# Kernel optimization log

Hardware: AMD Instinct MI355X
Metric: run time of the kernel (lower is better)

The kernel has to match this reference:

```python
import jax, jax.numpy as jnp
import numpy as np

DIM = 2048
N_HEADS = 16
Q_RANK = 1536
KV_RANK = 512
D_NOPE = 128
D_ROPE = 64
D_V = 128
EPS = 1e-6
B, S = 2, 2048
ROPE_THETA = 10000.0


def rmsnorm(x, w, eps=EPS):
    return x * jax.lax.rsqrt(jnp.mean(x * x, axis=-1, keepdims=True) + eps) * w


def apply_rope(x):
    # x: [b, h, s, d] with d even; LLaMA-style interleaved pair rotation
    b, h, s, d = x.shape
    inv_freq = 1.0 / (ROPE_THETA ** (jnp.arange(0, d, 2, dtype=jnp.float32) / d))
    ang = jnp.arange(s, dtype=jnp.float32)[:, None] * inv_freq[None, :]  # [s, d/2]
    cos, sin = jnp.cos(ang), jnp.sin(ang)
    xr = x.reshape(b, h, s, d // 2, 2)
    x1, x2 = xr[..., 0], xr[..., 1]
    o1 = x1 * cos - x2 * sin
    o2 = x1 * sin + x2 * cos
    return jnp.stack([o1, o2], axis=-1).reshape(b, h, s, d)


def setup_inputs() -> dict:
    key = jax.random.key(0)
    ks = jax.random.split(key, 10)
    std = 0.02
    return {
        "x": jax.random.normal(ks[0], (B, S, DIM), dtype=jnp.float32),
        "wq_down": jax.random.normal(ks[1], (Q_RANK, DIM), dtype=jnp.float32) * std,
        "q_norm_w": jnp.ones((Q_RANK,), dtype=jnp.float32),
        "wq_up": jax.random.normal(ks[2], (N_HEADS * D_NOPE, Q_RANK), dtype=jnp.float32) * std,
        "wq_rope": jax.random.normal(ks[3], (N_HEADS * D_ROPE, Q_RANK), dtype=jnp.float32) * std,
        "wkv_down": jax.random.normal(ks[4], (KV_RANK, DIM), dtype=jnp.float32) * std,
        "kv_norm_w": jnp.ones((KV_RANK,), dtype=jnp.float32),
        "wkv_up": jax.random.normal(ks[5], (N_HEADS * (D_NOPE + D_V), KV_RANK), dtype=jnp.float32) * std,
        "wk_rope": jax.random.normal(ks[6], (D_ROPE, DIM), dtype=jnp.float32) * std,
        "wo": jax.random.normal(ks[7], (DIM, N_HEADS * D_V), dtype=jnp.float32) * std,
    }


def reference(x, wq_down, q_norm_w, wq_up, wq_rope, wkv_down, kv_norm_w, wkv_up, wk_rope, wo):
    bs, s, _ = x.shape
    # low-rank Q path
    q_c = rmsnorm(x @ wq_down.T, q_norm_w)                              # [b,s,qr]
    q_nope = (q_c @ wq_up.T).reshape(bs, s, N_HEADS, D_NOPE).transpose(0, 2, 1, 3)
    q_pe = (q_c @ wq_rope.T).reshape(bs, s, N_HEADS, D_ROPE).transpose(0, 2, 1, 3)
    # low-rank KV path
    kv_c = rmsnorm(x @ wkv_down.T, kv_norm_w)                           # [b,s,kvr]
    kv_up = (kv_c @ wkv_up.T).reshape(bs, s, N_HEADS, D_NOPE + D_V)
    k_nope = kv_up[..., :D_NOPE].transpose(0, 2, 1, 3)                  # [b,h,s,dn]
    v = kv_up[..., D_NOPE:].transpose(0, 2, 1, 3)                       # [b,h,s,dv]
    # shared rope key (1 head), broadcast across heads
    k_rope = (x @ wk_rope.T).reshape(bs, s, 1, D_ROPE).transpose(0, 2, 1, 3)  # [b,1,s,dr]
    q_pe = apply_rope(q_pe)
    k_rope = apply_rope(k_rope)
    q = jnp.concatenate([q_nope, q_pe], axis=-1)                        # [b,h,s,dn+dr]
    k = jnp.concatenate([k_nope, jnp.broadcast_to(k_rope, (bs, N_HEADS, s, D_ROPE))], axis=-1)
    scale = 1.0 / np.sqrt(D_NOPE + D_ROPE)
    scores = jnp.einsum('bhqd,bhkd->bhqk', q, k) * scale                # [b,h,s,s]
    causal = jnp.tril(jnp.ones((s, s), dtype=bool))
    scores = jnp.where(causal, scores, -jnp.inf)
    probs = jax.nn.softmax(scores, axis=-1)
    out = jnp.einsum('bhqk,bhkv->bhqv', probs, v)                       # [b,h,s,dv]
    out = out.transpose(0, 2, 1, 3).reshape(bs, s, N_HEADS * D_V)
    return out @ wo.T
```

## Files before the change

### kernel.cpp

```cpp
#include <hip/hip_runtime.h>
#include <stdint.h>

typedef _Float16 f16x8 __attribute__((ext_vector_type(8)));
typedef _Float16 f16x4 __attribute__((ext_vector_type(4)));
typedef float fx4 __attribute__((ext_vector_type(4)));

static constexpr int S_LEN = 2048;
static constexpr int BATCH = 2;
static constexpr int TOKENS = BATCH * S_LEN;
static constexpr int DIM = 2048;
static constexpr int NH = 16;
static constexpr int QR = 1536;
static constexpr int KVR = 512;
static constexpr int DN = 128;
static constexpr int DR = 64;
static constexpr int DV = 128;

__device__ __forceinline__ void async16(const _Float16* g, _Float16* lds_base_uniform) {
  __builtin_amdgcn_global_load_lds(
      (const __attribute__((address_space(1))) void*)g,
      (__attribute__((address_space(3))) void*)lds_base_uniform, 16, 0, 0);
}

__device__ __forceinline__ void bar() {
  asm volatile("" ::: "memory");
  __builtin_amdgcn_s_barrier();
  asm volatile("" ::: "memory");
}
#define VMWAIT(n) asm volatile("s_waitcnt vmcnt(" #n ")" ::: "memory")

#define ROR16(x, ctrl) \
  __uint_as_float(__builtin_amdgcn_update_dpp(__float_as_uint(x), __float_as_uint(x), \
                                              (ctrl), 0xF, 0xF, false))

__device__ __forceinline__ void sincos_rev(float ang, float* sn, float* cs) {
  float rev = ang * 0.15915494309189535f;
  rev -= floorf(rev);
  *sn = __builtin_amdgcn_sinf(rev);
  *cs = __builtin_amdgcn_cosf(rev);
}

struct CvtSegs {
  const float* src[8];
  _Float16* dst[8];
  const float* nw[8];
  int nmod[8];
  int n4[8];
  int cum[9];
};
__global__ __launch_bounds__(256) void cvt_all(CvtSegs s) {
  const int b = blockIdx.x;
  int seg = 0;
#pragma unroll
  for (int k = 0; k < 7; ++k) seg += (b >= s.cum[seg + 1]) ? 1 : 0;
  const int i = (b - s.cum[seg]) * 256 + threadIdx.x;
  if (i >= s.n4[seg]) return;
  fx4 v = *(const fx4*)(s.src[seg] + (size_t)i * 4);
  if (s.nw[seg]) {
    const int c0 = (int)(((size_t)i * 4) % (size_t)s.nmod[seg]);
    fx4 wv = *(const fx4*)(s.nw[seg] + c0);
    v[0] *= wv[0]; v[1] *= wv[1]; v[2] *= wv[2]; v[3] *= wv[3];
  }
  f16x4 o;
  o[0] = (_Float16)v[0]; o[1] = (_Float16)v[1];
  o[2] = (_Float16)v[2]; o[3] = (_Float16)v[3];
  *(f16x4*)(s.dst[seg] + (size_t)i * 4) = o;
}

template <int MODE>
__global__ __launch_bounds__(256) void gemm_nt(const _Float16* __restrict__ A,
                                               const _Float16* __restrict__ W,
                                               void* __restrict__ C0v,
                                               void* __restrict__ C1v,
                                               void* __restrict__ C2v,
                                               int M, int N, int K) {
  __shared__ __attribute__((aligned(16))) _Float16 As[3][128 * 32];
  __shared__ __attribute__((aligned(16))) _Float16 Ws[3][128 * 32];
  const int tid = threadIdx.x;
  const int lane = tid & 63;
  const int wave = tid >> 6;
  const int wr = (wave >> 1) * 64;
  const int wc = (wave & 1) * 64;
  const int m16 = lane & 15;
  const int quad = lane >> 4;
  const int m0 = blockIdx.y * 128;
  const int n0 = blockIdx.x * 128;

  auto stage = [&](int buf, int k0) {
#pragma unroll
    for (int p = 0; p < 2; ++p) {
      const int cb = p * 256 + wave * 64;
      const int ch = cb + lane;
      const int r = ch >> 2;
      const int c8 = (ch & 3) * 8;
      async16(A + (size_t)(m0 + r) * K + k0 + c8, &As[buf][cb * 8]);
      async16(W + (size_t)(n0 + r) * K + k0 + c8, &Ws[buf][cb * 8]);
    }
  };

  const fx4 fz = {0.f, 0.f, 0.f, 0.f};
  fx4 acc[4][4];
#pragma unroll
  for (int i = 0; i < 4; ++i)
#pragma unroll
    for (int j = 0; j < 4; ++j) acc[i][j] = fz;

  const int nkt = K >> 5;
  stage(0, 0);
  stage(1, 32);
  int cur = 0;
  for (int kt = 0; kt < nkt; ++kt) {
    if (kt + 1 < nkt) { VMWAIT(4); } else { VMWAIT(0); }
    bar();
    if (kt + 2 < nkt) {
      int b2 = cur + 2; if (b2 >= 3) b2 -= 3;
      stage(b2, (kt + 2) * 32);
    }
    const _Float16* as = As[cur];
    const _Float16* ws = Ws[cur];
    f16x8 af[4], wf[4];
#pragma unroll
    for (int i = 0; i < 4; ++i)
      af[i] = *(const f16x8*)(&as[(wr + i * 16 + m16) * 32 + quad * 8]);
#pragma unroll
    for (int j = 0; j < 4; ++j)
      wf[j] = *(const f16x8*)(&ws[(wc + j * 16 + m16) * 32 + quad * 8]);
#pragma unroll
    for (int i = 0; i < 4; ++i)
#pragma unroll
      for (int j = 0; j < 4; ++j)
        acc[i][j] = __builtin_amdgcn_mfma_f32_16x16x32_f16(af[i], wf[j], acc[i][j], 0, 0, 0);
    if (++cur == 3) cur = 0;
  }

#pragma unroll
  for (int j = 0; j < 4; ++j) {
    const int col = n0 + wc + j * 16 + m16;
    if (MODE == 5) {
      if (col < 2048) {
#pragma unroll
        for (int i = 0; i < 4; ++i)
#pragma unroll
          for (int r = 0; r < 4; ++r) {
            const size_t row = (size_t)(m0 + wr + i * 16 + quad * 4 + r);
            const _Float16 v = (_Float16)acc[i][j][r];
            if (col < 1536) ((_Float16*)C0v)[row * 1536 + col] = v;
            else            ((_Float16*)C1v)[row * 512 + col - 1536] = v;
          }
      } else if (col < 2112) {
        const int d = col - 2048;
        const int pidx = d >> 1;
        const bool odd = (d & 1);
        const float fr = exp2f(-(float)pidx * 0.4152410118609203f);
#pragma unroll
        for (int i = 0; i < 4; ++i)
#pragma unroll
          for (int r = 0; r < 4; ++r) {
            const size_t row = (size_t)(m0 + wr + i * 16 + quad * 4 + r);
            const int spos = (int)(row & (S_LEN - 1));
            float sn, cs;
            sincos_rev((float)spos * fr, &sn, &cs);
            const float own = acc[i][j][r];
            const float oth = __shfl_xor(own, 1);
            const float res = odd ? (oth * sn + own * cs) : (own * cs - oth * sn);
            ((_Float16*)C2v)[row * 64 + d] = (_Float16)res;
          }
      }
    } else {
      if (col < N) {
#pragma unroll
        for (int i = 0; i < 4; ++i)
#pragma unroll
          for (int r = 0; r < 4; ++r) {
            const size_t row = (size_t)(m0 + wr + i * 16 + quad * 4 + r);
            ((float*)C0v)[row * N + col] = acc[i][j][r];
          }
      }
    }
  }
}

__global__ __launch_bounds__(256) void gemm_up(
    const _Float16* __restrict__ qc, const _Float16* __restrict__ wqu,
    const _Float16* __restrict__ kvc, const _Float16* __restrict__ wkvu,
    _Float16* __restrict__ qnope, _Float16* __restrict__ qpe,
    _Float16* __restrict__ knope, _Float16* __restrict__ vT) {
  __shared__ __attribute__((aligned(16))) _Float16 As[3][128 * 32];
  __shared__ __attribute__((aligned(16))) _Float16 Ws[3][128 * 32];
  const int tid = threadIdx.x;
  const int lane = tid & 63;
  const int wave = tid >> 6;
  const int wr = (wave >> 1) * 64;
  const int wc = (wave & 1) * 64;
  const int m16 = lane & 15;
  const int quad = lane >> 4;
  const int m0 = blockIdx.y * 128;
  const bool isq = (blockIdx.x < 24);
  const int n0 = (isq ? blockIdx.x : blockIdx.x - 24) * 128;
  const _Float16* A = isq ? qc : kvc;
  const _Float16* W = isq ? wqu : wkvu;
  const int K = isq ? QR : KVR;

  auto stage = [&](int buf, int k0) {
#pragma unroll
    for (int p = 0; p < 2; ++p) {
      const int cb = p * 256 + wave * 64;
      const int ch = cb + lane;
      const int r = ch >> 2;
      const int c8 = (ch & 3) * 8;
      async16(A + (size_t)(m0 + r) * K + k0 + c8, &As[buf][cb * 8]);
      async16(W + (size_t)(n0 + r) * K + k0 + c8, &Ws[buf][cb * 8]);
    }
  };

  const fx4 fz = {0.f, 0.f, 0.f, 0.f};
  fx4 acc[4][4];
#pragma unroll
  for (int i = 0; i < 4; ++i)
#pragma unroll
    for (int j = 0; j < 4; ++j) acc[i][j] = fz;
  float ssq[4] = {0.f, 0.f, 0.f, 0.f};

  const int nkt = K >> 5;
  stage(0, 0);
  stage(1, 32);
  int cur = 0;
  for (int kt = 0; kt < nkt; ++kt) {
    if (kt + 1 < nkt) { VMWAIT(4); } else { VMWAIT(0); }
    bar();
    if (kt + 2 < nkt) {
      int b2 = cur + 2; if (b2 >= 3) b2 -= 3;
      stage(b2, (kt + 2) * 32);
    }
    const _Float16* as = As[cur];
    const _Float16* ws = Ws[cur];
    f16x8 af[4], wf[4];
#pragma unroll
    for (int i = 0; i < 4; ++i)
      af[i] = *(const f16x8*)(&as[(wr + i * 16 + m16) * 32 + quad * 8]);
#pragma unroll
    for (int j = 0; j < 4; ++j)
      wf[j] = *(const f16x8*)(&ws[(wc + j * 16 + m16) * 32 + quad * 8]);
#pragma unroll
    for (int i = 0; i < 4; ++i)
#pragma unroll
      for (int j = 0; j < 4; ++j)
        acc[i][j] = __builtin_amdgcn_mfma_f32_16x16x32_f16(af[i], wf[j], acc[i][j], 0, 0, 0);
#pragma unroll
    for (int i = 0; i < 4; ++i) {
      float s0 = 0.f;
#pragma unroll
      for (int e = 0; e < 8; ++e) { const float xv = (float)af[i][e]; s0 += xv * xv; }
      ssq[i] += s0;
    }
    if (++cur == 3) cur = 0;
  }

  const float invK = 1.0f / (float)K;
  float rsq[4][4];
#pragma unroll
  for (int i = 0; i < 4; ++i) {
    float ss = ssq[i];
    ss += __shfl_xor(ss, 16);
    ss += __shfl_xor(ss, 32);
    const float rv = rsqrtf(ss * invK + 1e-6f);
#pragma unroll
    for (int r = 0; r < 4; ++r) rsq[i][r] = __shfl(rv, quad * 4 + r);
  }

#pragma unroll
  for (int j = 0; j < 4; ++j) {
    const int col = n0 + wc + j * 16 + m16;
    if (isq) {
#pragma unroll
      for (int i = 0; i < 4; ++i)
#pragma unroll
        for (int r = 0; r < 4; ++r) {
          const size_t row = (size_t)(m0 + wr + i * 16 + quad * 4 + r);
          const _Float16 v = (_Float16)(acc[i][j][r] * rsq[i][r]);
          if (col < 2048) qnope[row * 2048 + col] = v;
          else qpe[row * 1024 + col - 2048] = v;
        }
    } else {
      const int head = col >> 8;
      const int sub = col & 255;
      if (sub < 128) {
#pragma unroll
        for (int i = 0; i < 4; ++i)
#pragma unroll
          for (int r = 0; r < 4; ++r)
            knope[(size_t)(m0 + wr + i * 16 + quad * 4 + r) * 2048 + head * 128 + sub] =
                (_Float16)(acc[i][j][r] * rsq[i][r]);
      } else {
        const int dv = sub - 128;
#pragma unroll
        for (int i = 0; i < 4; ++i) {
          f16x4 v;
#pragma unroll
          for (int r = 0; r < 4; ++r) v[r] = (_Float16)(acc[i][j][r] * rsq[i][r]);
          *(f16x4*)(&vT[(size_t)(head * 128 + dv) * TOKENS + m0 + wr + i * 16 + quad * 4]) = v;
        }
      }
    }
  }
}

__global__ __launch_bounds__(512, 2) void mla_attn(
    const _Float16* __restrict__ qn,
    const _Float16* __restrict__ qp,
    const _Float16* __restrict__ kn,
    const _Float16* __restrict__ kr,
    const _Float16* __restrict__ vT,
    _Float16* __restrict__ out)
{
  __shared__ __attribute__((aligned(16))) _Float16 Ks[2][768 * 8];
  __shared__ __attribute__((aligned(16))) _Float16 Vs[2][512 * 8];
  __shared__ __attribute__((aligned(16))) _Float16 Ps[8][16][40];

  const int bid = blockIdx.x;
  const int j = bid >> 5;
  const int bh = bid & 31;
  const int b = bh >> 4;
  const int h = bh & 15;
  const int q16 = 15 - j;
  const int qb = q16 * 128;
  const int tok0 = b * S_LEN;

  const int tid = threadIdx.x;
  const int lane = tid & 63;
  const int wave = tid >> 6;
  const int m16 = lane & 15;
  const int quad = lane >> 4;
  const int R0 = qb + wave * 16;

  auto stageKV = [&](int buf, int kbase) {
#pragma unroll
    for (int jj = 0; jj < 3; ++jj) {
      const int idx = wave * 3 + jj;
      if (idx < 12) {
        const int ch = idx * 2 + (lane >> 5);
        const int key = lane & 31;
        const _Float16* g = (ch < 16)
            ? kn + (size_t)(tok0 + kbase + key) * 2048 + h * 128 + ch * 8
            : kr + (size_t)(tok0 + kbase + key) * 64 + (ch - 16) * 8;
        async16(g, &Ks[buf][idx * 512]);
      } else if (idx < 20) {
        const int iv = idx - 12;
        const int p = iv * 64 + lane;
        const int L = p ^ ((p >> 3) & 3);
        const int dv = L >> 2;
        const int qcc = L & 3;
        async16(vT + (size_t)(h * 128 + dv) * TOKENS + tok0 + kbase + qcc * 8,
                &Vs[buf][iv * 512]);
      }
    }
  };

  const float scale2 = 0.07216878364870323f * 1.4426950408889634f;
  const fx4 fz = {0.f, 0.f, 0.f, 0.f};

  f16x8 qf[6];
  {
    const int srow = qb + wave * 16 + m16;
    const size_t t = (size_t)(tok0 + srow);
#pragma unroll
    for (int kk = 0; kk < 4; ++kk)
      qf[kk] = *(const f16x8*)(qn + t * 2048 + h * 128 + kk * 32 + quad * 8);
#pragma unroll
    for (int kk = 0; kk < 2; ++kk) {
      f16x8 v = *(const f16x8*)(qp + t * 1024 + h * 64 + kk * 32 + quad * 8);
      f16x8 o;
      const int i0 = kk * 16 + quad * 4;
#pragma unroll
      for (int jj = 0; jj < 4; ++jj) {
        const float ang = (float)srow * exp2f(-(float)(i0 + jj) * 0.4152410118609203f);
        float sn, cs;
        sincos_rev(ang, &sn, &cs);
        const float x1 = (float)v[2 * jj], x2 = (float)v[2 * jj + 1];
        o[2 * jj]     = (_Float16)(x1 * cs - x2 * sn);
        o[2 * jj + 1] = (_Float16)(x1 * sn + x2 * cs);
      }
      qf[4 + kk] = o;
    }
  }

  fx4 oacc[9];
#pragma unroll
  for (int n = 0; n < 9; ++n) oacc[n] = fz;
  float mst[4];
#pragma unroll
  for (int r = 0; r < 4; ++r) mst[r] = -3.0e38f;
  f16x8 vones;
#pragma unroll
  for (int e = 0; e < 8; ++e) vones[e] = (_Float16)1.0f;

  const int nkt = (qb >> 5) + 4;

  stageKV(0, 0);
  for (int kt = 0; kt < nkt; ++kt) {
    const int kbase = kt * 32;
    __syncthreads();
    if (kt + 1 < nkt) stageKV((kt + 1) & 1, kbase + 32);

    const bool live = (kbase <= R0 + 15);
    if (!live) continue;
    const _Float16* ks = Ks[kt & 1];
    const _Float16* vs = Vs[kt & 1];

    fx4 sc[2];
    sc[0] = fz; sc[1] = fz;
    __builtin_amdgcn_s_setprio(1);
#pragma unroll
    for (int kk = 0; kk < 6; ++kk) {
#pragma unroll
      for (int n = 0; n < 2; ++n) {
        f16x8 kf = *(const f16x8*)(&ks[(kk * 128 + quad * 32 + n * 16 + m16) * 8]);
        sc[n] = __builtin_amdgcn_mfma_f32_16x16x32_f16(qf[kk], kf, sc[n], 0, 0, 0);
      }
    }
    __builtin_amdgcn_s_setprio(0);

    f16x8 vf[8];
#pragma unroll
    for (int n8 = 0; n8 < 8; ++n8) {
      const int c0 = (n8 * 16 + m16) * 4 + quad;
      vf[n8] = *(const f16x8*)(&vs[(c0 ^ ((c0 >> 3) & 3)) * 8]);
    }

    const bool needmask = (kbase + 31 > R0);
    float alpha[4];
    bool any_upd = false;
#pragma unroll
    for (int r = 0; r < 4; ++r) {
      float v0 = sc[0][r] * scale2;
      float v1 = sc[1][r] * scale2;
      if (needmask) {
        const int qrow = R0 + quad * 4 + r;
        if (kbase + m16 > qrow)      v0 = -3.0e38f;
        if (kbase + 16 + m16 > qrow) v1 = -3.0e38f;
      }
      const float pre = fmaxf(v0, v1);
      float al = 1.0f;
      if (__any(pre > mst[r] + 10.0f)) {
        float mx = pre;
        mx = fmaxf(mx, ROR16(mx, 0x128));
        mx = fmaxf(mx, ROR16(mx, 0x124));
        mx = fmaxf(mx, ROR16(mx, 0x122));
        mx = fmaxf(mx, ROR16(mx, 0x121));
        const float mn = fmaxf(mst[r], mx);
        al = exp2f(mst[r] - mn);
        mst[r] = mn;
        any_upd = true;
      }
      alpha[r] = al;
      const float p0 = exp2f(v0 - mst[r]);
      const float p1 = exp2f(v1 - mst[r]);
      _Float16* pr = &Ps[wave][quad * 4 + r][0];
      pr[m16] = (_Float16)p0;
      pr[16 + m16] = (_Float16)p1;
    }
    if (any_upd) {
#pragma unroll
      for (int n8 = 0; n8 < 9; ++n8)
#pragma unroll
        for (int r = 0; r < 4; ++r) oacc[n8][r] *= alpha[r];
    }

    f16x8 pf = *(const f16x8*)(&Ps[wave][m16][quad * 8]);
    __builtin_amdgcn_s_setprio(1);
#pragma unroll
    for (int n8 = 0; n8 < 8; ++n8)
      oacc[n8] = __builtin_amdgcn_mfma_f32_16x16x32_f16(pf, vf[n8], oacc[n8], 0, 0, 0);
    oacc[8] = __builtin_amdgcn_mfma_f32_16x16x32_f16(pf, vones, oacc[8], 0, 0, 0);
    __builtin_amdgcn_s_setprio(0);
  }

  float inv[4];
#pragma unroll
  for (int r = 0; r < 4; ++r) inv[r] = 1.0f / oacc[8][r];
#pragma unroll
  for (int n8 = 0; n8 < 8; ++n8) {
#pragma unroll
    for (int r = 0; r < 4; ++r) {
      const size_t t = (size_t)(tok0 + qb + wave * 16 + quad * 4 + r);
      out[t * 2048 + h * 128 + n8 * 16 + m16] = (_Float16)(oacc[n8][r] * inv[r]);
    }
  }
}

extern "C" void kernel_launch(void* const* d_in, const int* in_sizes, int n_in,
                              void* d_out, int out_size, void* d_ws, size_t ws_size,
                              hipStream_t stream) {
  const float* x         = (const float*)d_in[0];
  const float* wq_down   = (const float*)d_in[1];
  const float* q_norm_w  = (const float*)d_in[2];
  const float* wq_up     = (const float*)d_in[3];
  const float* wq_rope   = (const float*)d_in[4];
  const float* wkv_down  = (const float*)d_in[5];
  const float* kv_norm_w = (const float*)d_in[6];
  const float* wkv_up    = (const float*)d_in[7];
  const float* wk_rope   = (const float*)d_in[8];
  const float* wo        = (const float*)d_in[9];
  float* out = (float*)d_out;

  char* ws = (char*)d_ws;
  size_t off = 0;
  auto alloc = [&](size_t bytes) {
    char* p = ws + off;
    off += (bytes + 255) & ~(size_t)255;
    return p;
  };
  _Float16* x_h     = (_Float16*)alloc((size_t)TOKENS * DIM * 2);
  _Float16* wA_h    = (_Float16*)alloc((size_t)2176 * DIM * 2);
  _Float16* wquqr_h = (_Float16*)alloc((size_t)3072 * QR * 2);
  _Float16* wkvu_h  = (_Float16*)alloc((size_t)NH * 256 * KVR * 2);
  _Float16* wo_h    = (_Float16*)alloc((size_t)DIM * NH * DV * 2);
  _Float16* qc_h    = (_Float16*)alloc((size_t)TOKENS * QR * 2);
  _Float16* kvc_h   = (_Float16*)alloc((size_t)TOKENS * KVR * 2);
  _Float16* qnope_h = (_Float16*)alloc((size_t)TOKENS * 2048 * 2);
  _Float16* qpe_h   = (_Float16*)alloc((size_t)TOKENS * 1024 * 2);
  _Float16* knope_h = (_Float16*)alloc((size_t)TOKENS * 2048 * 2);
  _Float16* vT_h    = (_Float16*)alloc((size_t)2048 * TOKENS * 2);
  _Float16* krope_h = (_Float16*)alloc((size_t)TOKENS * DR * 2);
  _Float16* attn_h  = (_Float16*)alloc((size_t)TOKENS * 2048 * 2);

  CvtSegs cs;
  const float* srcs[8] = {x, wq_down, wq_up, wq_rope, wkv_down, wk_rope, wkv_up, wo};
  _Float16* dsts[8] = {x_h, wA_h, wquqr_h, wquqr_h + (size_t)2048 * QR,
                       wA_h + (size_t)1536 * DIM, wA_h + (size_t)2048 * DIM,
                       wkvu_h, wo_h};
  const float* nws[8] = {nullptr, nullptr, q_norm_w, q_norm_w, nullptr, nullptr,
                         kv_norm_w, nullptr};
  const int nmods[8] = {4, 4, QR, QR, 4, 4, KVR, 4};
  const size_t ns[8] = {(size_t)TOKENS * DIM, (size_t)QR * DIM, (size_t)2048 * QR,
                        (size_t)1024 * QR, (size_t)KVR * DIM, (size_t)DR * DIM,
                        (size_t)NH * 256 * KVR, (size_t)DIM * NH * DV};
  int cum = 0;
  for (int i = 0; i < 8; ++i) {
    cs.src[i] = srcs[i];
    cs.dst[i] = dsts[i];
    cs.nw[i] = nws[i];
    cs.nmod[i] = nmods[i];
    cs.n4[i] = (int)(ns[i] / 4);
    cs.cum[i] = cum;
    cum += (cs.n4[i] + 255) / 256;
  }
  cs.cum[8] = cum;
  cvt_all<<<dim3(cum), 256, 0, stream>>>(cs);

  const unsigned gm = TOKENS / 128;

  gemm_nt<5><<<dim3(17, gm), 256, 0, stream>>>(x_h, wA_h, qc_h, kvc_h, krope_h,
                                               TOKENS, 2112, DIM);
  gemm_up<<<dim3(24 + 32, gm), 256, 0, stream>>>(qc_h, wquqr_h, kvc_h, wkvu_h,
                                                 qnope_h, qpe_h, knope_h, vT_h);
  mla_attn<<<dim3(512), 512, 0, stream>>>(qnope_h, qpe_h, knope_h, krope_h, vT_h, attn_h);
  gemm_nt<1><<<dim3(16, gm), 256, 0, stream>>>(attn_h, wo_h, out, nullptr, nullptr,
                                               TOKENS, DIM, NH * DV);
}
```

Measured before the change: 472.4 us.

## Swizzle GEMM LDS tiles, precompute RMS norms, raise attention occupancy

The GEMM kernels now XOR-swizzle the 16-byte chunk index when staging A/W tiles into LDS and when reading fragments. This is meant to cut LDS bank conflicts on the fragment reads. The per-row sum-of-squares for the RMSNorm, which gemm_up used to recompute redundantly in every N-block, moves into a separate small rownorm kernel whose results gemm_up reads in its epilogue. The attention kernel's launch bounds ask for 4 blocks per CU instead of 2, which forces a tighter register budget and may cause spills.

After: 544.6 us. +15.3%, slower.

```diff
diff --git a/kernel.cpp b/kernel.cpp
--- a/kernel.cpp
+++ b/kernel.cpp
@@ -65,6 +65,30 @@
   o[0] = (_Float16)v[0]; o[1] = (_Float16)v[1];
   o[2] = (_Float16)v[2]; o[3] = (_Float16)v[3];
   *(f16x4*)(s.dst[seg] + (size_t)i * 4) = o;
+}
+
+__global__ __launch_bounds__(256) void rownorm(const _Float16* __restrict__ qc,
+                                               const _Float16* __restrict__ kvc,
+                                               float* __restrict__ rq,
+                                               float* __restrict__ rkv) {
+  const int idx = blockIdx.x * 4 + (threadIdx.x >> 6);
+  const int lane = threadIdx.x & 63;
+  const bool isq = idx < TOKENS;
+  const int row = isq ? idx : idx - TOKENS;
+  const int NC = isq ? QR : KVR;
+  const f16x8* p = (const f16x8*)((isq ? qc : kvc) + (size_t)row * NC);
+  float ss = 0.f;
+  for (int c = lane; c < NC / 8; c += 64) {
+    f16x8 v = p[c];
+#pragma unroll
+    for (int e = 0; e < 8; ++e) { const float x = (float)v[e]; ss += x * x; }
+  }
+#pragma unroll
+  for (int d = 1; d < 64; d <<= 1) ss += __shfl_xor(ss, d);
+  if (lane == 0) {
+    const float rv = rsqrtf(ss / (float)NC + 1e-6f);
+    if (isq) rq[row] = rv; else rkv[row] = rv;
+  }
 }
 
 template <int MODE>
@@ -83,6 +107,7 @@
   const int wc = (wave & 1) * 64;
   const int m16 = lane & 15;
   const int quad = lane >> 4;
+  const int swz = (m16 >> 1) & 3;
   const int m0 = blockIdx.y * 128;
   const int n0 = blockIdx.x * 128;
 
@@ -92,7 +117,7 @@
       const int cb = p * 256 + wave * 64;
       const int ch = cb + lane;
       const int r = ch >> 2;
-      const int c8 = (ch & 3) * 8;
+      const int c8 = ((ch & 3) ^ ((r >> 1) & 3)) * 8;
       async16(A + (size_t)(m0 + r) * K + k0 + c8, &As[buf][cb * 8]);
       async16(W + (size_t)(n0 + r) * K + k0 + c8, &Ws[buf][cb * 8]);
     }
@@ -121,10 +146,10 @@
     f16x8 af[4], wf[4];
 #pragma unroll
     for (int i = 0; i < 4; ++i)
-      af[i] = *(const f16x8*)(&as[(wr + i * 16 + m16) * 32 + quad * 8]);
+      af[i] = *(const f16x8*)(&as[((wr + i * 16 + m16) * 4 + (quad ^ swz)) * 8]);
 #pragma unroll
     for (int j = 0; j < 4; ++j)
-      wf[j] = *(const f16x8*)(&ws[(wc + j * 16 + m16) * 32 + quad * 8]);
+      wf[j] = *(const f16x8*)(&ws[((wc + j * 16 + m16) * 4 + (quad ^ swz)) * 8]);
 #pragma unroll
     for (int i = 0; i < 4; ++i)
 #pragma unroll
@@ -183,6 +208,7 @@
 __global__ __launch_bounds__(256) void gemm_up(
     const _Float16* __restrict__ qc, const _Float16* __restrict__ wqu,
     const _Float16* __restrict__ kvc, const _Float16* __restrict__ wkvu,
+    const float* __restrict__ rq, const float* __restrict__ rkv,
     _Float16* __restrict__ qnope, _Float16* __restrict__ qpe,
     _Float16* __restrict__ knope, _Float16* __restrict__ vT) {
   __shared__ __attribute__((aligned(16))) _Float16 As[3][128 * 32];
@@ -194,6 +220,7 @@
   const int wc = (wave & 1) * 64;
   const int m16 = lane & 15;
   const int quad = lane >> 4;
+  const int swz = (m16 >> 1) & 3;
   const int m0 = blockIdx.y * 128;
   const bool isq = (blockIdx.x < 24);
   const int n0 = (isq ? blockIdx.x : blockIdx.x - 24) * 128;
@@ -207,7 +234,7 @@
       const int cb = p * 256 + wave * 64;
       const int ch = cb + lane;
       const int r = ch >> 2;
-      const int c8 = (ch & 3) * 8;
+      const int c8 = ((ch & 3) ^ ((r >> 1) & 3)) * 8;
       async16(A + (size_t)(m0 + r) * K + k0 + c8, &As[buf][cb * 8]);
       async16(W + (size_t)(n0 + r) * K + k0 + c8, &Ws[buf][cb * 8]);
     }
@@ -219,7 +246,6 @@
   for (int i = 0; i < 4; ++i)
 #pragma unroll
     for (int j = 0; j < 4; ++j) acc[i][j] = fz;
-  float ssq[4] = {0.f, 0.f, 0.f, 0.f};
 
   const int nkt = K >> 5;
   stage(0, 0);
@@ -237,36 +263,25 @@
     f16x8 af[4], wf[4];
 #pragma unroll
     for (int i = 0; i < 4; ++i)
-      af[i] = *(const f16x8*)(&as[(wr + i * 16 + m16) * 32 + quad * 8]);
+      af[i] = *(const f16x8*)(&as[((wr + i * 16 + m16) * 4 + (quad ^ swz)) * 8]);
 #pragma unroll
     for (int j = 0; j < 4; ++j)
-      wf[j] = *(const f16x8*)(&ws[(wc + j * 16 + m16) * 32 + quad * 8]);
+      wf[j] = *(const f16x8*)(&ws[((wc + j * 16 + m16) * 4 + (quad ^ swz)) * 8]);
 #pragma unroll
     for (int i = 0; i < 4; ++i)
 #pragma unroll
       for (int j = 0; j < 4; ++j)
         acc[i][j] = __builtin_amdgcn_mfma_f32_16x16x32_f16(af[i], wf[j], acc[i][j], 0, 0, 0);
-#pragma unroll
-    for (int i = 0; i < 4; ++i) {
-      float s0 = 0.f;
-#pragma unroll
-      for (int e = 0; e < 8; ++e) { const float xv = (float)af[i][e]; s0 += xv * xv; }
-      ssq[i] += s0;
-    }
     if (++cur == 3) cur = 0;
   }
 
-  const float invK = 1.0f / (float)K;
+  const float* rs = isq ? rq : rkv;
   float rsq[4][4];
 #pragma unroll
-  for (int i = 0; i < 4; ++i) {
-    float ss = ssq[i];
-    ss += __shfl_xor(ss, 16);
-    ss += __shfl_xor(ss, 32);
-    const float rv = rsqrtf(ss * invK + 1e-6f);
-#pragma unroll
-    for (int r = 0; r < 4; ++r) rsq[i][r] = __shfl(rv, quad * 4 + r);
-  }
+  for (int i = 0; i < 4; ++i)
+#pragma unroll
+    for (int r = 0; r < 4; ++r)
+      rsq[i][r] = rs[m0 + wr + i * 16 + quad * 4 + r];
 
 #pragma unroll
   for (int j = 0; j < 4; ++j) {
@@ -305,7 +320,7 @@
   }
 }
 
-__global__ __launch_bounds__(512, 2) void mla_attn(
+__global__ __launch_bounds__(512, 4) void mla_attn(
     const _Float16* __restrict__ qn,
     const _Float16* __restrict__ qp,
     const _Float16* __restrict__ kn,
@@ -523,6 +538,8 @@
   _Float16* vT_h    = (_Float16*)alloc((size_t)2048 * TOKENS * 2);
   _Float16* krope_h = (_Float16*)alloc((size_t)TOKENS * DR * 2);
   _Float16* attn_h  = (_Float16*)alloc((size_t)TOKENS * 2048 * 2);
+  float* rq_h       = (float*)alloc((size_t)TOKENS * 4);
+  float* rkv_h      = (float*)alloc((size_t)TOKENS * 4);
 
   CvtSegs cs;
   const float* srcs[8] = {x, wq_down, wq_up, wq_rope, wkv_down, wk_rope, wkv_up, wo};
@@ -552,7 +569,9 @@
 
   gemm_nt<5><<<dim3(17, gm), 256, 0, stream>>>(x_h, wA_h, qc_h, kvc_h, krope_h,
                                                TOKENS, 2112, DIM);
+  rownorm<<<dim3(2 * TOKENS / 4), 256, 0, stream>>>(qc_h, kvc_h, rq_h, rkv_h);
   gemm_up<<<dim3(24 + 32, gm), 256, 0, stream>>>(qc_h, wquqr_h, kvc_h, wkvu_h,
+                                                 rq_h, rkv_h,
                                                  qnope_h, qpe_h, knope_h, vT_h);
   mla_attn<<<dim3(512), 512, 0, stream>>>(qnope_h, qpe_h, knope_h, krope_h, vT_h, attn_h);
   gemm_nt<1><<<dim3(16, gm), 256, 0, stream>>>(attn_h, wo_h, out, nullptr, nullptr,
```
